# Kernel optimization log

Hardware: AMD Instinct MI355X
Metric: run time of the kernel (lower is better)

The kernel has to match this reference:

```python
import math
import jax, jax.numpy as jnp
import numpy as np

B, Q, K, D = 16, 2048, 2048, 128

def setup_inputs() -> dict:
    key = jax.random.key(0)
    kq, kk, kv, kl = jax.random.split(key, 4)
    queries = jax.random.normal(kq, (B, Q, D), dtype=jnp.float32)
    keys = jax.random.normal(kk, (B, K, D), dtype=jnp.float32)
    values = jax.random.normal(kv, (B, K, D), dtype=jnp.float32)
    valid_lens = jax.random.randint(kl, (B,), 0, K, dtype=jnp.int64)
    return {"queries": queries, "keys": keys, "values": values, "valid_lens": valid_lens}

def reference(queries, keys, values, valid_lens):
    d = queries.shape[-1]
    # [B, Q, K] scores
    scores = jnp.einsum("bqd,bkd->bqk", queries, keys) / math.sqrt(d)
    # Original masks X[index][length:] = -1e6, i.e. along the QUERY axis (dim 1),
    # filling entire rows; softmax over the key axis then yields uniform weights
    # for those rows. Reproduce exactly.
    q_idx = jnp.arange(queries.shape[1])  # [Q]
    mask = q_idx[None, :, None] >= valid_lens[:, None, None]  # [B, Q, 1]
    scores = jnp.where(mask, jnp.float32(-1000000.0), scores)
    attention_weights = jax.nn.softmax(scores, axis=-1)
    # dropout p=0.0 (eval) -> identity
    return jnp.einsum("bqk,bkd->bqd", attention_weights, values)
```

## Files before the change

kernel.cpp:

```cpp
#include <hip/hip_runtime.h>
#include <math.h>


#define Bn 16
#define Qn 2048
#define Kn 2048
#define Dn 128
#define SCALE 0.08838834764831845f

typedef _Float16 f16;
typedef _Float16 f16x8_t __attribute__((ext_vector_type(8)));
typedef float f32x16_t __attribute__((ext_vector_type(16)));

typedef __attribute__((address_space(1))) const unsigned int glb_u32;
typedef __attribute__((address_space(3))) unsigned int lds_u32;

__device__ __forceinline__ void g2l16(const void* g, void* l) {
  __builtin_amdgcn_global_load_lds((glb_u32*)g, (lds_u32*)l, 16, 0, 0);
}


__global__ void __launch_bounds__(256) prep_kernel(
    const float* __restrict__ Qg, const float* __restrict__ Kg,
    const float* __restrict__ Vg, f16* __restrict__ Qh, f16* __restrict__ Kh,
    f16* __restrict__ Vt, float* __restrict__ sv) {
  __shared__ float ps[8][32];
  const int b = blockIdx.z;
  const int x = threadIdx.x, y = threadIdx.y;

  {
    const int lb = (b * 4 + blockIdx.y) * 32 + blockIdx.x;
    const int t = y * 32 + x;
    const size_t key = (size_t)lb * 16 + (t >> 4);
    const int G = t & 15;
    const float* kp = Kg + (key << 7) + G * 8;
    float4 f0 = *(const float4*)kp;
    float4 f1 = *(const float4*)(kp + 4);
    f16x8_t o;
    o[0] = (f16)f0.x; o[1] = (f16)f0.y; o[2] = (f16)f0.z; o[3] = (f16)f0.w;
    o[4] = (f16)f1.x; o[5] = (f16)f1.y; o[6] = (f16)f1.z; o[7] = (f16)f1.w;
    const int gs = (G & 8) | ((G & 7) ^ ((int)key & 7));
    *(f16x8_t*)(Kh + (key << 7) + (gs << 3)) = o;

    const float* qp = Qg + (key << 7) + G * 8;
    float4 q0 = *(const float4*)qp;
    float4 q1 = *(const float4*)(qp + 4);
    f16x8_t oq;
    oq[0] = (f16)q0.x; oq[1] = (f16)q0.y; oq[2] = (f16)q0.z; oq[3] = (f16)q0.w;
    oq[4] = (f16)q1.x; oq[5] = (f16)q1.y; oq[6] = (f16)q1.z; oq[7] = (f16)q1.w;
    *(f16x8_t*)(Qh + (key << 7) + G * 8) = oq;
  }

  const int k0 = blockIdx.x * 64, d0 = blockIdx.y * 32;
  const int d = d0 + x;
  const float* vp = Vg + ((size_t)b * Kn + k0 + y * 8) * Dn + d;
  float s = 0.f;
  f16x8_t gr;
#pragma unroll
  for (int j = 0; j < 8; j++) {
    float v = vp[(size_t)j * Dn];
    s += v;
    gr[j] = (f16)v;
  }
  {
    const int kb = k0 >> 6;
    const int G = y;
    const int gs = G ^ (d & 7);
    *(f16x8_t*)(Vt + (((size_t)(b * (Kn / 64) + kb) * 128 + d) << 6) + (gs << 3)) = gr;
  }

  ps[y][x] = s;
  __syncthreads();
  if (y == 0) {
    float tot = 0.f;
#pragma unroll
    for (int j = 0; j < 8; j++) tot += ps[j][x];
    atomicAdd(&sv[b * Dn + d0 + x], tot);
  }
}

__device__ __forceinline__ int load_vl(const int* __restrict__ vlp, int b) {
  bool is64 = true;
#pragma unroll
  for (int i = 1; i < 16; i += 2) is64 = is64 && (vlp[i] == 0);
  return is64 ? vlp[2 * b] : vlp[b];
}


__global__ void __launch_bounds__(256, 2) flash_sp(
    const f16* __restrict__ Qh, const f16* __restrict__ Kh,
    const f16* __restrict__ Vt, const int* __restrict__ vlp,
    const float* __restrict__ sv, float* __restrict__ Out) {
  const int b = blockIdx.x;
  const int qt = blockIdx.y;
  const int q0 = qt << 7;
  const int vl = load_vl(vlp, b);
  const int tid = threadIdx.x;

  if (q0 >= vl) {
    const float invK = 1.0f / (float)Kn;
    const int row = tid >> 1, h = tid & 1;
    const float4* svp = (const float4*)(sv + b * Dn + h * 64);
    float4* op = (float4*)(Out + ((size_t)b * Qn + q0 + row) * Dn + h * 64);
#pragma unroll
    for (int i = 0; i < 16; i++) {
      float4 s4 = svp[i];
      op[i] = make_float4(s4.x * invK, s4.y * invK, s4.z * invK, s4.w * invK);
    }
    return;
  }

  __shared__ __align__(16) f16 Ks[2][64 * 128];
  __shared__ __align__(16) f16 Vs[2][128 * 64];

  const int wave = tid >> 6, lane = tid & 63;
  const int H = lane >> 5, l5 = lane & 31;
  const int qbase = q0 + wave * 32;
  const bool wact = qbase < vl;
  const int q_lane = qbase + l5;
  const float sc = (q_lane >= vl) ? 0.f : SCALE;

  const int krow = (l5 & 0x13) | ((l5 & 4) << 1) | ((l5 & 8) >> 1);
  const int krow7 = krow & 7;

  f16x8_t qf[8];
  if (wact) {
    const f16* qp = Qh + ((size_t)b * Qn + q_lane) * Dn + 8 * H;
#pragma unroll
    for (int s = 0; s < 8; s++) qf[s] = *(const f16x8_t*)(qp + 16 * s);
  }

  f32x16_t O[4];
#pragma unroll
  for (int i = 0; i < 4; i++) O[i] = (f32x16_t)(0.f);
  float l_lane = 0.f;

  const char* KgT = (const char*)Kh + ((size_t)b * Kn << 8);
  const char* VgT = (const char*)Vt + ((size_t)(b * (Kn / 64)) << 14);

  {
    const char* kg = KgT + wave * 4096 + lane * 16;
    const char* vg = VgT + wave * 4096 + lane * 16;
    f16* kl = Ks[0] + wave * 2048;
    f16* vli = Vs[0] + wave * 2048;
#pragma unroll
    for (int i = 0; i < 4; i++) {
      g2l16(kg + i * 1024, kl + i * 512);
      g2l16(vg + i * 1024, vli + i * 512);
    }
  }
  __syncthreads();

  int buf = 0;
  for (int sl = 0; sl < 32; sl++) {
    if (sl < 31) {
      const char* kg = KgT + (size_t)(sl + 1) * 16384 + wave * 4096 + lane * 16;
      const char* vg = VgT + (size_t)(sl + 1) * 16384 + wave * 4096 + lane * 16;
      f16* kl = Ks[buf ^ 1] + wave * 2048;
      f16* vli = Vs[buf ^ 1] + wave * 2048;
#pragma unroll
      for (int i = 0; i < 4; i++) {
        g2l16(kg + i * 1024, kl + i * 512);
        g2l16(vg + i * 1024, vli + i * 512);
      }
    }

    if (wact) {
#pragma unroll
      for (int sub = 0; sub < 2; sub++) {
        f32x16_t T = (f32x16_t)(0.f);
        const f16* krp = Ks[buf] + ((sub * 32 + krow) << 7);
#pragma unroll
        for (int s = 0; s < 8; s++) {
          const int G = 2 * s + H;
          const int gs = (G & 8) | ((G & 7) ^ krow7);
          f16x8_t kf = *(const f16x8_t*)(krp + (gs << 3));
          T = __builtin_amdgcn_mfma_f32_32x32x16_f16(kf, qf[s], T, 0, 0, 0);
        }

        f16x8_t pf0, pf1;
        float ls = 0.f;
#pragma unroll
        for (int r = 0; r < 8; r++) {
          float p = __expf(T[r] * sc);
          ls += p;
          pf0[r] = (f16)p;
        }
#pragma unroll
        for (int r = 8; r < 16; r++) {
          float p = __expf(T[r] * sc);
          ls += p;
          pf1[r - 8] = (f16)p;
        }
        l_lane += ls;

#pragma unroll
        for (int dt = 0; dt < 4; dt++) {
          const f16* vrp = Vs[buf] + ((dt * 32 + l5) << 6);
          const int G0 = sub * 4 + H, G1 = sub * 4 + 2 + H;
          const int gs0 = G0 ^ (l5 & 7);
          const int gs1 = G1 ^ (l5 & 7);
          f16x8_t vf0 = *(const f16x8_t*)(vrp + (gs0 << 3));
          f16x8_t vf1 = *(const f16x8_t*)(vrp + (gs1 << 3));
          O[dt] = __builtin_amdgcn_mfma_f32_32x32x16_f16(pf0, vf0, O[dt], 0, 0, 0);
          O[dt] = __builtin_amdgcn_mfma_f32_32x32x16_f16(pf1, vf1, O[dt], 0, 0, 0);
        }
      }
    }
    __syncthreads();
    buf ^= 1;
  }

  float* op = Out + ((size_t)b * Qn + qbase) * Dn;
  if (wact) {
    float ll = l_lane + __shfl_xor(l_lane, 32);
    float inv[16];
#pragma unroll
    for (int r = 0; r < 16; r++) {
      const int qrow = (r & 3) + 8 * (r >> 2) + 4 * H;
      inv[r] = 1.0f / __shfl(ll, qrow);
    }
#pragma unroll
    for (int dt = 0; dt < 4; dt++) {
#pragma unroll
      for (int r = 0; r < 16; r++) {
        const int qrow = (r & 3) + 8 * (r >> 2) + 4 * H;
        op[(size_t)qrow * Dn + dt * 32 + l5] = O[dt][r] * inv[r];
      }
    }
  } else {
    const float invK = 1.0f / (float)Kn;
#pragma unroll
    for (int dt = 0; dt < 4; dt++) {
      const float svv = sv[b * Dn + dt * 32 + l5] * invK;
#pragma unroll
      for (int r = 0; r < 16; r++) {
        const int qrow = (r & 3) + 8 * (r >> 2) + 4 * H;
        op[(size_t)qrow * Dn + dt * 32 + l5] = svv;
      }
    }
  }
}


extern "C" void kernel_launch(void* const* d_in, const int* in_sizes, int n_in,
                              void* d_out, int out_size, void* d_ws, size_t ws_size,
                              hipStream_t stream) {
  const float* Qg = (const float*)d_in[0];
  const float* Kg = (const float*)d_in[1];
  const float* Vg = (const float*)d_in[2];
  const int* vl = (const int*)d_in[3];
  float* Out = (float*)d_out;

  char* ws = (char*)d_ws;
  const size_t kv = (size_t)Bn * Kn * Dn * 2;
  float* sumV = (float*)ws;
  f16* Kh = (f16*)(ws + 8192);
  f16* Vt = (f16*)(ws + 8192 + kv);
  f16* Qh = (f16*)(ws + 8192 + 2 * kv);

  hipMemsetAsync(sumV, 0, Bn * Dn * sizeof(float), stream);

  prep_kernel<<<dim3(32, 4, Bn), dim3(32, 8), 0, stream>>>(
      Qg, Kg, Vg, Qh, Kh, Vt, sumV);
  flash_sp<<<dim3(Bn, 16), 256, 0, stream>>>(Qh, Kh, Vt, vl, sumV, Out);
}
```

Baseline: 148.6 us.

## Split key dimension across four segments with a separate combine kernel

Adds a split-K flash variant that processes a quarter of the keys per block, grid z = 4, and writes fp16 partial outputs and row sums to workspace. A combine kernel sums the partials, normalises them, and fills masked rows with the mean of V. The aim is to quadruple the grid so the GPU is better filled, since many query tiles are skipped by valid_lens. The cost is an extra kernel launch, partial-output traffic, and fp16 rounding of the unnormalised partials. The new path is used only if the workspace is large enough, otherwise the old kernel runs.

```diff
diff --git a/kernel.cpp b/kernel.cpp
--- a/kernel.cpp
+++ b/kernel.cpp
@@ -87,6 +87,136 @@
 }
 
 
+__global__ void __launch_bounds__(256, 2) flash4(
+    const f16* __restrict__ Qh, const f16* __restrict__ Kh,
+    const f16* __restrict__ Vt, const int* __restrict__ vlp,
+    f16* __restrict__ Po, float* __restrict__ Lb) {
+  const int b = blockIdx.x;
+  const int qt = blockIdx.y;
+  const int seg = blockIdx.z;
+  const int q0 = qt << 7;
+  const int vl = load_vl(vlp, b);
+  if (q0 >= vl) return;
+
+  __shared__ __align__(16) f16 Ks[2][64 * 128];
+  __shared__ __align__(16) f16 Vs[2][128 * 64];
+
+  const int tid = threadIdx.x;
+  const int wave = tid >> 6, lane = tid & 63;
+  const int H = lane >> 5, l5 = lane & 31;
+  const int qbase = q0 + wave * 32;
+  const bool wact = qbase < vl;
+  const int q_lane = qbase + l5;
+  const float sc = (q_lane >= vl) ? 0.f : SCALE;
+
+  const int krow = (l5 & 0x13) | ((l5 & 4) << 1) | ((l5 & 8) >> 1);
+  const int krow7 = krow & 7;
+
+  f16x8_t qf[8];
+  if (wact) {
+    const f16* qp = Qh + ((size_t)b * Qn + q_lane) * Dn + 8 * H;
+#pragma unroll
+    for (int s = 0; s < 8; s++) qf[s] = *(const f16x8_t*)(qp + 16 * s);
+  }
+
+  f32x16_t O[4];
+#pragma unroll
+  for (int i = 0; i < 4; i++) O[i] = (f32x16_t)(0.f);
+  float l_lane = 0.f;
+
+  const char* KgT = (const char*)Kh + (((size_t)b * Kn + seg * 512) << 8);
+  const char* VgT = (const char*)Vt + ((size_t)(b * (Kn / 64) + seg * 8) << 14);
+
+  {
+    const char* kg = KgT + wave * 4096 + lane * 16;
+    const char* vg = VgT + wave * 4096 + lane * 16;
+    f16* kl = Ks[0] + wave * 2048;
+    f16* vli = Vs[0] + wave * 2048;
+#pragma unroll
+    for (int i = 0; i < 4; i++) {
+      g2l16(kg + i * 1024, kl + i * 512);
+      g2l16(vg + i * 1024, vli + i * 512);
+    }
+  }
+  __syncthreads();
+
+  int buf = 0;
+  for (int sl = 0; sl < 8; sl++) {
+    if (sl < 7) {
+      const char* kg = KgT + (size_t)(sl + 1) * 16384 + wave * 4096 + lane * 16;
+      const char* vg = VgT + (size_t)(sl + 1) * 16384 + wave * 4096 + lane * 16;
+      f16* kl = Ks[buf ^ 1] + wave * 2048;
+      f16* vli = Vs[buf ^ 1] + wave * 2048;
+#pragma unroll
+      for (int i = 0; i < 4; i++) {
+        g2l16(kg + i * 1024, kl + i * 512);
+        g2l16(vg + i * 1024, vli + i * 512);
+      }
+    }
+
+    if (wact) {
+#pragma unroll
+      for (int sub = 0; sub < 2; sub++) {
+        f32x16_t T = (f32x16_t)(0.f);
+        const f16* krp = Ks[buf] + ((sub * 32 + krow) << 7);
+#pragma unroll
+        for (int s = 0; s < 8; s++) {
+          const int G = 2 * s + H;
+          const int gs = (G & 8) | ((G & 7) ^ krow7);
+          f16x8_t kf = *(const f16x8_t*)(krp + (gs << 3));
+          T = __builtin_amdgcn_mfma_f32_32x32x16_f16(kf, qf[s], T, 0, 0, 0);
+        }
+
+        f16x8_t pf0, pf1;
+        float ls = 0.f;
+#pragma unroll
+        for (int r = 0; r < 8; r++) {
+          float p = __expf(T[r] * sc);
+          ls += p;
+          pf0[r] = (f16)p;
+        }
+#pragma unroll
+        for (int r = 8; r < 16; r++) {
+          float p = __expf(T[r] * sc);
+          ls += p;
+          pf1[r - 8] = (f16)p;
+        }
+        l_lane += ls;
+
+#pragma unroll
+        for (int dt = 0; dt < 4; dt++) {
+          const f16* vrp = Vs[buf] + ((dt * 32 + l5) << 6);
+          const int G0 = sub * 4 + H, G1 = sub * 4 + 2 + H;
+          const int gs0 = G0 ^ (l5 & 7);
+          const int gs1 = G1 ^ (l5 & 7);
+          f16x8_t vf0 = *(const f16x8_t*)(vrp + (gs0 << 3));
+          f16x8_t vf1 = *(const f16x8_t*)(vrp + (gs1 << 3));
+          O[dt] = __builtin_amdgcn_mfma_f32_32x32x16_f16(pf0, vf0, O[dt], 0, 0, 0);
+          O[dt] = __builtin_amdgcn_mfma_f32_32x32x16_f16(pf1, vf1, O[dt], 0, 0, 0);
+        }
+      }
+    }
+    __syncthreads();
+    buf ^= 1;
+  }
+
+  if (!wact) return;
+
+  float ll = l_lane + __shfl_xor(l_lane, 32);
+  if (lane < 32) Lb[(size_t)(seg * Bn + b) * Qn + qbase + l5] = ll;
+
+  f16* po = Po + ((size_t)(seg * Bn + b) * Qn + qbase) * Dn;
+#pragma unroll
+  for (int dt = 0; dt < 4; dt++) {
+#pragma unroll
+    for (int r = 0; r < 16; r++) {
+      const int qrow = (r & 3) + 8 * (r >> 2) + 4 * H;
+      po[(size_t)qrow * Dn + dt * 32 + l5] = (f16)O[dt][r];
+    }
+  }
+}
+
+
 __global__ void __launch_bounds__(256, 2) flash_sp(
     const f16* __restrict__ Qh, const f16* __restrict__ Kh,
     const f16* __restrict__ Vt, const int* __restrict__ vlp,
@@ -177,7 +307,6 @@
           f16x8_t kf = *(const f16x8_t*)(krp + (gs << 3));
           T = __builtin_amdgcn_mfma_f32_32x32x16_f16(kf, qf[s], T, 0, 0, 0);
         }
-
         f16x8_t pf0, pf1;
         float ls = 0.f;
 #pragma unroll
@@ -193,7 +322,6 @@
           pf1[r - 8] = (f16)p;
         }
         l_lane += ls;
-
 #pragma unroll
         for (int dt = 0; dt < 4; dt++) {
           const f16* vrp = Vs[buf] + ((dt * 32 + l5) << 6);
@@ -243,6 +371,61 @@
 }
 
 
+template <int S>
+__global__ void __launch_bounds__(256) combine_kernel(
+    const f16* __restrict__ Po, const float* __restrict__ Lb,
+    const float* __restrict__ sv, const int* __restrict__ vlp,
+    float* __restrict__ Out) {
+  const int b = blockIdx.y, q0 = blockIdx.x * 64;
+  const int vl = load_vl(vlp, b);
+  const int tid = threadIdx.x;
+
+  __shared__ float linv[64];
+  if (tid < 64) {
+    float s = 0.f;
+#pragma unroll
+    for (int sg = 0; sg < S; sg++) s += Lb[(size_t)(sg * Bn + b) * Qn + q0 + tid];
+    linv[tid] = 1.0f / s;
+  }
+  __syncthreads();
+
+  const int row16 = tid >> 4;
+  const int d8 = (tid & 15) * 8;
+  const float invK = 1.0f / (float)Kn;
+  float mv[8];
+#pragma unroll
+  for (int j = 0; j < 8; j++) mv[j] = sv[b * Dn + d8 + j] * invK;
+
+#pragma unroll
+  for (int pass = 0; pass < 4; pass++) {
+    const int row = pass * 16 + row16;
+    const int q = q0 + row;
+    float acc[8];
+    if (q >= vl) {
+#pragma unroll
+      for (int j = 0; j < 8; j++) acc[j] = mv[j];
+    } else {
+#pragma unroll
+      for (int j = 0; j < 8; j++) acc[j] = 0.f;
+#pragma unroll
+      for (int sg = 0; sg < S; sg++) {
+        f16x8_t v = *(const f16x8_t*)(Po + ((size_t)(sg * Bn + b) * Qn + q) * Dn + d8);
+#pragma unroll
+        for (int j = 0; j < 8; j++) acc[j] += (float)v[j];
+      }
+      const float li = linv[row];
+#pragma unroll
+      for (int j = 0; j < 8; j++) acc[j] *= li;
+    }
+    float4 o0 = make_float4(acc[0], acc[1], acc[2], acc[3]);
+    float4 o1 = make_float4(acc[4], acc[5], acc[6], acc[7]);
+    float* op = Out + ((size_t)b * Qn + q) * Dn + d8;
+    *(float4*)op = o0;
+    *(float4*)(op + 4) = o1;
+  }
+}
+
+
 extern "C" void kernel_launch(void* const* d_in, const int* in_sizes, int n_in,
                               void* d_out, int out_size, void* d_ws, size_t ws_size,
                               hipStream_t stream) {
@@ -259,9 +442,23 @@
   f16* Vt = (f16*)(ws + 8192 + kv);
   f16* Qh = (f16*)(ws + 8192 + 2 * kv);
 
+  const size_t plane = (size_t)Bn * Qn * Dn * 2;
+  const size_t lplane = (size_t)Bn * Qn * 4;
+  const size_t base = 8192 + 3 * kv;
+  const size_t need4 = base + 4 * plane + 4 * lplane;
+  const size_t need1 = base;
+
   hipMemsetAsync(sumV, 0, Bn * Dn * sizeof(float), stream);
 
   prep_kernel<<<dim3(32, 4, Bn), dim3(32, 8), 0, stream>>>(
       Qg, Kg, Vg, Qh, Kh, Vt, sumV);
-  flash_sp<<<dim3(Bn, 16), 256, 0, stream>>>(Qh, Kh, Vt, vl, sumV, Out);
-}
+
+  if (ws_size >= need4) {
+    f16* Po = (f16*)(ws + base);
+    float* Lb = (float*)(ws + base + 4 * plane);
+    flash4<<<dim3(Bn, 16, 4), 256, 0, stream>>>(Qh, Kh, Vt, vl, Po, Lb);
+    combine_kernel<4><<<dim3(Qn / 64, Bn), 256, 0, stream>>>(Po, Lb, sumV, vl, Out);
+  } else {
+    flash_sp<<<dim3(Bn, 16), 256, 0, stream>>>(Qh, Kh, Vt, vl, sumV, Out);
+  }
+}
```

Result: faster. 141.9 us (-4.5%).

## Split attention over key segments with direct global fragment loads and combine pass

Applied to the files above, without the earlier changes.

Splits the key dimension into up to four segments launched as separate blocks, each writing fp16 partial outputs and row sums that a new combine kernel reduces and normalizes. K and V are prepacked in an MFMA-fragment-ordered layout, so waves read operands directly from global memory instead of staging through LDS with double buffering and barriers. The Q conversion moves into the attention kernel, so the prep kernel no longer handles Q. This aims to raise occupancy and balance work across CUs when valid lengths are short. The cost is extra partial-output traffic, a third kernel launch, and fp16 rounding of the partial sums.

```diff
diff --git a/kernel.cpp b/kernel.cpp
--- a/kernel.cpp
+++ b/kernel.cpp
@@ -12,18 +12,10 @@
 typedef _Float16 f16x8_t __attribute__((ext_vector_type(8)));
 typedef float f32x16_t __attribute__((ext_vector_type(16)));
 
-typedef __attribute__((address_space(1))) const unsigned int glb_u32;
-typedef __attribute__((address_space(3))) unsigned int lds_u32;
-
-__device__ __forceinline__ void g2l16(const void* g, void* l) {
-  __builtin_amdgcn_global_load_lds((glb_u32*)g, (lds_u32*)l, 16, 0, 0);
-}
-
 
 __global__ void __launch_bounds__(256) prep_kernel(
-    const float* __restrict__ Qg, const float* __restrict__ Kg,
-    const float* __restrict__ Vg, f16* __restrict__ Qh, f16* __restrict__ Kh,
-    f16* __restrict__ Vt, float* __restrict__ sv) {
+    const float* __restrict__ Kg, const float* __restrict__ Vg,
+    f16* __restrict__ Kh, f16* __restrict__ Vt, float* __restrict__ sv) {
   __shared__ float ps[8][32];
   const int b = blockIdx.z;
   const int x = threadIdx.x, y = threadIdx.y;
@@ -39,16 +31,12 @@
     f16x8_t o;
     o[0] = (f16)f0.x; o[1] = (f16)f0.y; o[2] = (f16)f0.z; o[3] = (f16)f0.w;
     o[4] = (f16)f1.x; o[5] = (f16)f1.y; o[6] = (f16)f1.z; o[7] = (f16)f1.w;
-    const int gs = (G & 8) | ((G & 7) ^ ((int)key & 7));
-    *(f16x8_t*)(Kh + (key << 7) + (gs << 3)) = o;
-
-    const float* qp = Qg + (key << 7) + G * 8;
-    float4 q0 = *(const float4*)qp;
-    float4 q1 = *(const float4*)(qp + 4);
-    f16x8_t oq;
-    oq[0] = (f16)q0.x; oq[1] = (f16)q0.y; oq[2] = (f16)q0.z; oq[3] = (f16)q0.w;
-    oq[4] = (f16)q1.x; oq[5] = (f16)q1.y; oq[6] = (f16)q1.z; oq[7] = (f16)q1.w;
-    *(f16x8_t*)(Qh + (key << 7) + G * 8) = oq;
+    const int r32 = (int)key & 31;
+    const int l5k = (r32 & 0x13) | ((r32 & 4) << 1) | ((r32 & 8) >> 1);
+    f16* dst = Kh + ((key >> 5) << 12)
+                  + ((G >> 1) << 9)
+                  + (((G & 1) << 5) + l5k) * 8;
+    *(f16x8_t*)dst = o;
   }
 
   const int k0 = blockIdx.x * 64, d0 = blockIdx.y * 32;
@@ -64,9 +52,11 @@
   }
   {
     const int kb = k0 >> 6;
-    const int G = y;
-    const int gs = G ^ (d & 7);
-    *(f16x8_t*)(Vt + (((size_t)(b * (Kn / 64) + kb) * 128 + d) << 6) + (gs << 3)) = gr;
+    const int c = ((y >> 2) << 3) + ((d >> 5) << 1) + ((y >> 1) & 1);
+    f16* dst = Vt + (size_t)(b * (Kn / 64) + kb) * 8192
+                  + (c << 9)
+                  + (((y & 1) << 5) + (d & 31)) * 8;
+    *(f16x8_t*)dst = gr;
   }
 
   ps[y][x] = s;
@@ -87,47 +77,38 @@
 }
 
 
-__global__ void __launch_bounds__(256, 2) flash_sp(
-    const f16* __restrict__ Qh, const f16* __restrict__ Kh,
+template <int SEG>
+__global__ void __launch_bounds__(256, 2) flash_st(
+    const float* __restrict__ Qg, const f16* __restrict__ Kh,
     const f16* __restrict__ Vt, const int* __restrict__ vlp,
-    const float* __restrict__ sv, float* __restrict__ Out) {
+    f16* __restrict__ Po, float* __restrict__ Lb) {
   const int b = blockIdx.x;
   const int qt = blockIdx.y;
+  const int seg = blockIdx.z;
   const int q0 = qt << 7;
   const int vl = load_vl(vlp, b);
+  if (q0 >= vl) return;
+
   const int tid = threadIdx.x;
-
-  if (q0 >= vl) {
-    const float invK = 1.0f / (float)Kn;
-    const int row = tid >> 1, h = tid & 1;
-    const float4* svp = (const float4*)(sv + b * Dn + h * 64);
-    float4* op = (float4*)(Out + ((size_t)b * Qn + q0 + row) * Dn + h * 64);
-#pragma unroll
-    for (int i = 0; i < 16; i++) {
-      float4 s4 = svp[i];
-      op[i] = make_float4(s4.x * invK, s4.y * invK, s4.z * invK, s4.w * invK);
-    }
-    return;
-  }
-
-  __shared__ __align__(16) f16 Ks[2][64 * 128];
-  __shared__ __align__(16) f16 Vs[2][128 * 64];
-
   const int wave = tid >> 6, lane = tid & 63;
   const int H = lane >> 5, l5 = lane & 31;
   const int qbase = q0 + wave * 32;
-  const bool wact = qbase < vl;
+  if (qbase >= vl) return;
   const int q_lane = qbase + l5;
   const float sc = (q_lane >= vl) ? 0.f : SCALE;
 
-  const int krow = (l5 & 0x13) | ((l5 & 4) << 1) | ((l5 & 8) >> 1);
-  const int krow7 = krow & 7;
-
   f16x8_t qf[8];
-  if (wact) {
-    const f16* qp = Qh + ((size_t)b * Qn + q_lane) * Dn + 8 * H;
-#pragma unroll
-    for (int s = 0; s < 8; s++) qf[s] = *(const f16x8_t*)(qp + 16 * s);
+  {
+    const float* qp = Qg + ((size_t)b * Qn + q_lane) * Dn + 8 * H;
+#pragma unroll
+    for (int s = 0; s < 8; s++) {
+      float4 f0 = *(const float4*)(qp + 16 * s);
+      float4 f1 = *(const float4*)(qp + 16 * s + 4);
+      f16x8_t q8;
+      q8[0] = (f16)f0.x; q8[1] = (f16)f0.y; q8[2] = (f16)f0.z; q8[3] = (f16)f0.w;
+      q8[4] = (f16)f1.x; q8[5] = (f16)f1.y; q8[6] = (f16)f1.z; q8[7] = (f16)f1.w;
+      qf[s] = q8;
+    }
   }
 
   f32x16_t O[4];
@@ -135,110 +116,117 @@
   for (int i = 0; i < 4; i++) O[i] = (f32x16_t)(0.f);
   float l_lane = 0.f;
 
-  const char* KgT = (const char*)Kh + ((size_t)b * Kn << 8);
-  const char* VgT = (const char*)Vt + ((size_t)(b * (Kn / 64)) << 14);
-
-  {
-    const char* kg = KgT + wave * 4096 + lane * 16;
-    const char* vg = VgT + wave * 4096 + lane * 16;
-    f16* kl = Ks[0] + wave * 2048;
-    f16* vli = Vs[0] + wave * 2048;
-#pragma unroll
-    for (int i = 0; i < 4; i++) {
-      g2l16(kg + i * 1024, kl + i * 512);
-      g2l16(vg + i * 1024, vli + i * 512);
-    }
-  }
-  __syncthreads();
-
-  int buf = 0;
-  for (int sl = 0; sl < 32; sl++) {
-    if (sl < 31) {
-      const char* kg = KgT + (size_t)(sl + 1) * 16384 + wave * 4096 + lane * 16;
-      const char* vg = VgT + (size_t)(sl + 1) * 16384 + wave * 4096 + lane * 16;
-      f16* kl = Ks[buf ^ 1] + wave * 2048;
-      f16* vli = Vs[buf ^ 1] + wave * 2048;
-#pragma unroll
-      for (int i = 0; i < 4; i++) {
-        g2l16(kg + i * 1024, kl + i * 512);
-        g2l16(vg + i * 1024, vli + i * 512);
-      }
-    }
-
-    if (wact) {
-#pragma unroll
-      for (int sub = 0; sub < 2; sub++) {
-        f32x16_t T = (f32x16_t)(0.f);
-        const f16* krp = Ks[buf] + ((sub * 32 + krow) << 7);
-#pragma unroll
-        for (int s = 0; s < 8; s++) {
-          const int G = 2 * s + H;
-          const int gs = (G & 8) | ((G & 7) ^ krow7);
-          f16x8_t kf = *(const f16x8_t*)(krp + (gs << 3));
-          T = __builtin_amdgcn_mfma_f32_32x32x16_f16(kf, qf[s], T, 0, 0, 0);
-        }
-
-        f16x8_t pf0, pf1;
-        float ls = 0.f;
-#pragma unroll
-        for (int r = 0; r < 8; r++) {
-          float p = __expf(T[r] * sc);
-          ls += p;
-          pf0[r] = (f16)p;
-        }
-#pragma unroll
-        for (int r = 8; r < 16; r++) {
-          float p = __expf(T[r] * sc);
-          ls += p;
-          pf1[r - 8] = (f16)p;
-        }
-        l_lane += ls;
-
-#pragma unroll
-        for (int dt = 0; dt < 4; dt++) {
-          const f16* vrp = Vs[buf] + ((dt * 32 + l5) << 6);
-          const int G0 = sub * 4 + H, G1 = sub * 4 + 2 + H;
-          const int gs0 = G0 ^ (l5 & 7);
-          const int gs1 = G1 ^ (l5 & 7);
-          f16x8_t vf0 = *(const f16x8_t*)(vrp + (gs0 << 3));
-          f16x8_t vf1 = *(const f16x8_t*)(vrp + (gs1 << 3));
-          O[dt] = __builtin_amdgcn_mfma_f32_32x32x16_f16(pf0, vf0, O[dt], 0, 0, 0);
-          O[dt] = __builtin_amdgcn_mfma_f32_32x32x16_f16(pf1, vf1, O[dt], 0, 0, 0);
-        }
-      }
-    }
-    __syncthreads();
-    buf ^= 1;
-  }
-
-  float* op = Out + ((size_t)b * Qn + qbase) * Dn;
-  if (wact) {
-    float ll = l_lane + __shfl_xor(l_lane, 32);
-    float inv[16];
+  const int KSEG = Kn / SEG;
+  const f16* Kseg = Kh + ((size_t)(b * Kn + seg * KSEG) << 7);
+  const f16* Vseg = Vt + (size_t)(b * (Kn / 64) + seg * (KSEG / 64)) * 8192;
+  const int lslot = lane * 8;
+
+  for (int sl = 0; sl < KSEG / 64; sl++) {
+    const f16* Kt = Kseg + ((size_t)sl << 13);
+    const f16* Vtt = Vseg + ((size_t)sl << 13);
+#pragma unroll
+    for (int sub = 0; sub < 2; sub++) {
+      f32x16_t T = (f32x16_t)(0.f);
+      const f16* kcb = Kt + (sub << 12) + lslot;
+#pragma unroll
+      for (int s = 0; s < 8; s++) {
+        f16x8_t kf = *(const f16x8_t*)(kcb + (s << 9));
+        T = __builtin_amdgcn_mfma_f32_32x32x16_f16(kf, qf[s], T, 0, 0, 0);
+      }
+
+      f16x8_t pf0, pf1;
+      float ls = 0.f;
+#pragma unroll
+      for (int r = 0; r < 8; r++) {
+        float p = __expf(T[r] * sc);
+        ls += p;
+        pf0[r] = (f16)p;
+      }
+#pragma unroll
+      for (int r = 8; r < 16; r++) {
+        float p = __expf(T[r] * sc);
+        ls += p;
+        pf1[r - 8] = (f16)p;
+      }
+      l_lane += ls;
+
+#pragma unroll
+      for (int dt = 0; dt < 4; dt++) {
+        const f16* vcb = Vtt + (((sub << 3) + (dt << 1)) << 9) + lslot;
+        f16x8_t vf0 = *(const f16x8_t*)vcb;
+        f16x8_t vf1 = *(const f16x8_t*)(vcb + 512);
+        O[dt] = __builtin_amdgcn_mfma_f32_32x32x16_f16(pf0, vf0, O[dt], 0, 0, 0);
+        O[dt] = __builtin_amdgcn_mfma_f32_32x32x16_f16(pf1, vf1, O[dt], 0, 0, 0);
+      }
+    }
+  }
+
+  float ll = l_lane + __shfl_xor(l_lane, 32);
+  if (lane < 32) Lb[(size_t)(seg * Bn + b) * Qn + qbase + l5] = ll;
+
+  f16* po = Po + ((size_t)(seg * Bn + b) * Qn + qbase) * Dn;
+#pragma unroll
+  for (int dt = 0; dt < 4; dt++) {
 #pragma unroll
     for (int r = 0; r < 16; r++) {
       const int qrow = (r & 3) + 8 * (r >> 2) + 4 * H;
-      inv[r] = 1.0f / __shfl(ll, qrow);
-    }
-#pragma unroll
-    for (int dt = 0; dt < 4; dt++) {
-#pragma unroll
-      for (int r = 0; r < 16; r++) {
-        const int qrow = (r & 3) + 8 * (r >> 2) + 4 * H;
-        op[(size_t)qrow * Dn + dt * 32 + l5] = O[dt][r] * inv[r];
-      }
-    }
-  } else {
-    const float invK = 1.0f / (float)Kn;
-#pragma unroll
-    for (int dt = 0; dt < 4; dt++) {
-      const float svv = sv[b * Dn + dt * 32 + l5] * invK;
-#pragma unroll
-      for (int r = 0; r < 16; r++) {
-        const int qrow = (r & 3) + 8 * (r >> 2) + 4 * H;
-        op[(size_t)qrow * Dn + dt * 32 + l5] = svv;
-      }
-    }
+      po[(size_t)qrow * Dn + dt * 32 + l5] = (f16)O[dt][r];
+    }
+  }
+}
+
+
+template <int S>
+__global__ void __launch_bounds__(256) combine_kernel(
+    const f16* __restrict__ Po, const float* __restrict__ Lb,
+    const float* __restrict__ sv, const int* __restrict__ vlp,
+    float* __restrict__ Out) {
+  const int b = blockIdx.y, q0 = blockIdx.x * 64;
+  const int vl = load_vl(vlp, b);
+  const int tid = threadIdx.x;
+
+  __shared__ float linv[64];
+  if (tid < 64) {
+    float s = 0.f;
+#pragma unroll
+    for (int sg = 0; sg < S; sg++) s += Lb[(size_t)(sg * Bn + b) * Qn + q0 + tid];
+    linv[tid] = 1.0f / s;
+  }
+  __syncthreads();
+
+  const int row16 = tid >> 4;
+  const int d8 = (tid & 15) * 8;
+  const float invK = 1.0f / (float)Kn;
+  float mv[8];
+#pragma unroll
+  for (int j = 0; j < 8; j++) mv[j] = sv[b * Dn + d8 + j] * invK;
+
+#pragma unroll
+  for (int pass = 0; pass < 4; pass++) {
+    const int row = pass * 16 + row16;
+    const int q = q0 + row;
+    float acc[8];
+    if (q >= vl) {
+#pragma unroll
+      for (int j = 0; j < 8; j++) acc[j] = mv[j];
+    } else {
+#pragma unroll
+      for (int j = 0; j < 8; j++) acc[j] = 0.f;
+#pragma unroll
+      for (int sg = 0; sg < S; sg++) {
+        f16x8_t v = *(const f16x8_t*)(Po + ((size_t)(sg * Bn + b) * Qn + q) * Dn + d8);
+#pragma unroll
+        for (int j = 0; j < 8; j++) acc[j] += (float)v[j];
+      }
+      const float li = linv[row];
+#pragma unroll
+      for (int j = 0; j < 8; j++) acc[j] *= li;
+    }
+    float4 o0 = make_float4(acc[0], acc[1], acc[2], acc[3]);
+    float4 o1 = make_float4(acc[4], acc[5], acc[6], acc[7]);
+    float* op = Out + ((size_t)b * Qn + q) * Dn + d8;
+    *(float4*)op = o0;
+    *(float4*)(op + 4) = o1;
   }
 }
 
@@ -257,11 +245,27 @@
   float* sumV = (float*)ws;
   f16* Kh = (f16*)(ws + 8192);
   f16* Vt = (f16*)(ws + 8192 + kv);
-  f16* Qh = (f16*)(ws + 8192 + 2 * kv);
+
+  const size_t plane = (size_t)Bn * Qn * Dn * 2;
+  const size_t lplane = (size_t)Bn * Qn * 4;
+  const size_t base = 8192 + 2 * kv;
+  f16* Po = (f16*)(ws + base);
 
   hipMemsetAsync(sumV, 0, Bn * Dn * sizeof(float), stream);
 
-  prep_kernel<<<dim3(32, 4, Bn), dim3(32, 8), 0, stream>>>(
-      Qg, Kg, Vg, Qh, Kh, Vt, sumV);
-  flash_sp<<<dim3(Bn, 16), 256, 0, stream>>>(Qh, Kh, Vt, vl, sumV, Out);
-}
+  prep_kernel<<<dim3(32, 4, Bn), dim3(32, 8), 0, stream>>>(Kg, Vg, Kh, Vt, sumV);
+
+  if (ws_size >= base + 4 * (plane + lplane)) {
+    float* Lb = (float*)(ws + base + 4 * plane);
+    flash_st<4><<<dim3(Bn, 16, 4), 256, 0, stream>>>(Qg, Kh, Vt, vl, Po, Lb);
+    combine_kernel<4><<<dim3(Qn / 64, Bn), 256, 0, stream>>>(Po, Lb, sumV, vl, Out);
+  } else if (ws_size >= base + 2 * (plane + lplane)) {
+    float* Lb = (float*)(ws + base + 2 * plane);
+    flash_st<2><<<dim3(Bn, 16, 2), 256, 0, stream>>>(Qg, Kh, Vt, vl, Po, Lb);
+    combine_kernel<2><<<dim3(Qn / 64, Bn), 256, 0, stream>>>(Po, Lb, sumV, vl, Out);
+  } else {
+    float* Lb = (float*)(ws + base + 1 * plane);
+    flash_st<1><<<dim3(Bn, 16, 1), 256, 0, stream>>>(Qg, Kh, Vt, vl, Po, Lb);
+    combine_kernel<1><<<dim3(Qn / 64, Bn), 256, 0, stream>>>(Po, Lb, sumV, vl, Out);
+  }
+}
```

Result: slower. 228.6 us (+53.8%).
